# Optimization experiments

Hardware: AMD Instinct MI355X
Metric: run time of the kernel (lower is better)

Reference implementation:

```python
import jax, jax.numpy as jnp
import numpy as np
from jax import lax

B_, L_, D_ = 4, 2048, 256
DI, NS, DC, DTR = 512, 16, 4, 16  # d_inner=2*D, d_state, d_conv, dt_rank=ceil(D/16)
DFF = 4 * D_


def setup_inputs():
    key = jax.random.key(0)
    ks = jax.random.split(key, 20)
    rn = lambda k, s, sc=0.02: jax.random.normal(k, s, jnp.float32) * sc
    return {
        "x": jax.random.normal(ks[0], (B_, L_, D_), jnp.float32),
        "in_proj_w": rn(ks[1], (2 * DI, D_)), "in_proj_b": jnp.zeros((2 * DI,), jnp.float32),
        "conv_w": rn(ks[2], (DI, DC), 0.1), "conv_b": jnp.zeros((DI,), jnp.float32),
        "x_proj_w": rn(ks[3], (DTR + 2 * NS, DI)),
        "dt_proj_w": rn(ks[4], (DI, DTR), 0.1), "dt_proj_b": rn(ks[5], (DI,), 0.5),
        "A_log": jnp.log(jnp.tile(jnp.arange(1, NS + 1, dtype=jnp.float32), (DI, 1))),
        "D_ssm": jnp.ones((DI,), jnp.float32),
        "out_proj_w": rn(ks[6], (D_, DI)), "out_proj_b": jnp.zeros((D_,), jnp.float32),
        "ln1_g": jnp.ones((D_,), jnp.float32), "ln1_b": jnp.zeros((D_,), jnp.float32),
        "fc1_w": rn(ks[7], (DFF, D_)), "fc1_b": jnp.zeros((DFF,), jnp.float32),
        "fc2_w": rn(ks[8], (D_, DFF)), "fc2_b": jnp.zeros((D_,), jnp.float32),
        "ln2_g": jnp.ones((D_,), jnp.float32), "ln2_b": jnp.zeros((D_,), jnp.float32),
    }


def _layer_norm(x, g, b, eps=1e-5):
    m = jnp.mean(x, -1, keepdims=True)
    v = jnp.mean((x - m) ** 2, -1, keepdims=True)
    return (x - m) / jnp.sqrt(v + eps) * g + b


def _mamba(x, in_proj_w, in_proj_b, conv_w, conv_b, x_proj_w, dt_proj_w, dt_proj_b, A_log, D_ssm, out_proj_w, out_proj_b):
    B, L, D = x.shape
    xz = x @ in_proj_w.T + in_proj_b                       # [B,L,2*DI]
    xi, z = jnp.split(xz, 2, axis=-1)
    # causal depthwise conv over time
    xc = jnp.transpose(xi, (0, 2, 1))                       # [B,DI,L]
    xc = lax.conv_general_dilated(xc, conv_w[:, None, :], (1,), [(DC - 1, 0)],
                                  dimension_numbers=("NCH", "OIH", "NCH"),
                                  feature_group_count=DI)
    xi = jax.nn.silu(jnp.transpose(xc + conv_b[None, :, None], (0, 2, 1)))  # [B,L,DI]
    x_dbl = xi @ x_proj_w.T                                 # [B,L,DTR+2*NS]
    dt, Bs, Cs = jnp.split(x_dbl, [DTR, DTR + NS], axis=-1)
    dt = jax.nn.softplus(dt @ dt_proj_w.T + dt_proj_b)      # [B,L,DI]
    A = -jnp.exp(A_log)                                     # [DI,NS]
    dA = jnp.exp(dt[..., None] * A)                         # [B,L,DI,NS]
    dBu = dt[..., None] * Bs[:, :, None, :] * xi[..., None]  # [B,L,DI,NS]
    dA_t = jnp.moveaxis(dA, 1, 0)
    dBu_t = jnp.moveaxis(dBu, 1, 0)
    C_t = jnp.moveaxis(Cs, 1, 0)                            # [L,B,NS]

    def step(h, inp):
        a, bu, c = inp
        h = a * h + bu                                      # [B,DI,NS]
        y = jnp.einsum("bdn,bn->bd", h, c)
        return h, y

    h0 = jnp.zeros((B, DI, NS), x.dtype)
    _, ys = lax.scan(step, h0, (dA_t, dBu_t, C_t))
    y = jnp.moveaxis(ys, 0, 1) + xi * D_ssm                 # [B,L,DI]
    y = y * jax.nn.silu(z)
    return y @ out_proj_w.T + out_proj_b


def reference(x, in_proj_w, in_proj_b, conv_w, conv_b, x_proj_w, dt_proj_w, dt_proj_b,
              A_log, D_ssm, out_proj_w, out_proj_b, ln1_g, ln1_b, fc1_w, fc1_b,
              fc2_w, fc2_b, ln2_g, ln2_b):
    gelu = lambda t: jax.nn.gelu(t, approximate=False)
    ssm = _mamba(x, in_proj_w, in_proj_b, conv_w, conv_b, x_proj_w, dt_proj_w,
                 dt_proj_b, A_log, D_ssm, out_proj_w, out_proj_b)
    y = _layer_norm(x + ssm, ln1_g, ln1_b)                  # dropout = identity (eval)
    ffn = gelu(gelu(y @ fc1_w.T + fc1_b) @ fc2_w.T + fc2_b)
    return _layer_norm(y + ffn, ln2_g, ln2_b)
```

## Files before the change

kernel.cpp:

```cpp
#include <hip/hip_runtime.h>

typedef __bf16 bf16x8 __attribute__((ext_vector_type(8)));
typedef float  f32x4  __attribute__((ext_vector_type(4)));

#define AS1 __attribute__((address_space(1)))
#define AS3 __attribute__((address_space(3)))

__device__ __forceinline__ float bf2f(ushort u) {
    union { unsigned int i; float f; } v; v.i = ((unsigned int)u) << 16; return v.f;
}
__device__ __forceinline__ ushort f2bf(float f) {
    union { float f; unsigned int i; } v; v.f = f;
    unsigned int i = v.i;
    unsigned int r = i + 0x7FFFu + ((i >> 16) & 1u);
    return (ushort)(r >> 16);
}
__device__ __forceinline__ float bflo(unsigned int u) { return bf2f((ushort)(u & 0xFFFFu)); }
__device__ __forceinline__ float bfhi(unsigned int u) { return bf2f((ushort)(u >> 16)); }

__global__ void sniff_k(const ushort* __restrict__ x, int* __restrict__ flag)
{
    const int lane = threadIdx.x;
    int cnt = 0;
    #pragma unroll
    for (int r = 0; r < 4; r++) {
        const ushort u = x[lane + r * 64];
        const int e = (u >> 7) & 0xFF;
        if ((u & 0x7FFF) == 0 || (e >= 112 && e <= 141)) cnt++;
    }
    #pragma unroll
    for (int o = 32; o > 0; o >>= 1) cnt += __shfl_down(cnt, o);
    if (lane == 0) flag[0] = (cnt >= 224) ? 1 : 0;
}

struct CanonArgs {
    const void* src[20];
    int off[20];
    int total;
};

__launch_bounds__(256)
__global__ void canon_k(CanonArgs a, ushort* __restrict__ dst, const int* __restrict__ flag)
{
    const int i = blockIdx.x * 256 + threadIdx.x;
    if (i >= a.total) return;
    const int fl = flag[0];
    int s = 0;
    #pragma unroll
    for (int t = 1; t < 20; t++) if (i >= a.off[t]) s = t;
    const int li = i - a.off[s];
    ushort v;
    if (fl) v = ((const ushort*)a.src[s])[li];
    else    v = f2bf(((const float*)a.src[s])[li]);
    dst[i] = v;
}

__launch_bounds__(256)
__global__ void prep_k(const ushort* __restrict__ dtw, const ushort* __restrict__ xpw,
                       ushort* __restrict__ dtw_pad, ushort* __restrict__ xpw_pad)
{
    const int i = blockIdx.x * 256 + threadIdx.x;
    if (i < 16384) {
        const int dd = i >> 5, r = i & 31;
        dtw_pad[i] = (r < 16) ? dtw[dd * 16 + r] : (ushort)0;
    } else {
        const int j = i - 16384;
        const int r = j >> 9;
        xpw_pad[j] = (r < 48) ? xpw[j] : (ushort)0;
    }
}

template<int BM, int BN, int ACT, bool HASB, bool WF32, bool WBF16>
__launch_bounds__(256, 2)
__global__ void gemm_bt(const ushort* __restrict__ A, const ushort* __restrict__ W,
                        const ushort* __restrict__ bias,
                        float* __restrict__ Cf, ushort* __restrict__ Cb,
                        int M, int N, int K, int lda)
{
    constexpr int WMT = BM / 32;
    constexpr int WNT = BN / 32;
    __shared__ __align__(16) ushort As[BM * 32];
    __shared__ __align__(16) ushort Bs[BN * 32];
    const int tid  = threadIdx.x;
    const int wave = tid >> 6;
    const int lane = tid & 63;
    const int m0 = blockIdx.x * BM;
    const int n0 = blockIdx.y * BN;
    const int wm = (wave >> 1) * (BM / 2);
    const int wn = (wave & 1) * (BN / 2);
    const int lrow = lane & 15;
    const int quad = lane >> 4;

    f32x4 acc[WMT][WNT];
    #pragma unroll
    for (int i = 0; i < WMT; i++)
        #pragma unroll
        for (int j = 0; j < WNT; j++)
            #pragma unroll
            for (int r = 0; r < 4; r++) acc[i][j][r] = 0.f;

    for (int k0 = 0; k0 < K; k0 += 32) {
        #pragma unroll
        for (int t = 0; t < BM / 64; t++) {
            const int inst = t * 4 + wave;
            const int row  = inst * 16 + (lane >> 2);
            const int sub  = lane & 3;
            const ushort* gp = A + (size_t)(m0 + row) * lda + (k0 + sub * 8);
            __builtin_amdgcn_global_load_lds((AS1 void*)(void*)gp,
                                             (AS3 void*)(As + inst * 512), 16, 0, 0);
        }
        #pragma unroll
        for (int t = 0; t < BN / 64; t++) {
            const int inst = t * 4 + wave;
            const int row  = inst * 16 + (lane >> 2);
            const int sub  = lane & 3;
            const ushort* gp = W + (size_t)(n0 + row) * K + (k0 + sub * 8);
            __builtin_amdgcn_global_load_lds((AS1 void*)(void*)gp,
                                             (AS3 void*)(Bs + inst * 512), 16, 0, 0);
        }
        __syncthreads();

        bf16x8 afr[WMT], bfr[WNT];
        #pragma unroll
        for (int i = 0; i < WMT; i++)
            afr[i] = *(const bf16x8*)&As[(wm + i * 16 + lrow) * 32 + quad * 8];
        #pragma unroll
        for (int j = 0; j < WNT; j++)
            bfr[j] = *(const bf16x8*)&Bs[(wn + j * 16 + lrow) * 32 + quad * 8];
        #pragma unroll
        for (int i = 0; i < WMT; i++)
            #pragma unroll
            for (int j = 0; j < WNT; j++)
                acc[i][j] = __builtin_amdgcn_mfma_f32_16x16x32_bf16(afr[i], bfr[j], acc[i][j], 0, 0, 0);
        __syncthreads();
    }

    #pragma unroll
    for (int i = 0; i < WMT; i++) {
        const int gm = m0 + wm + i * 16 + quad * 4;
        #pragma unroll
        for (int j = 0; j < WNT; j++) {
            const int gn = n0 + wn + j * 16 + lrow;
            const float bv = HASB ? bf2f(bias[gn]) : 0.f;
            #pragma unroll
            for (int r = 0; r < 4; r++) {
                float v = acc[i][j][r] + bv;
                if (ACT == 1) v = 0.5f * v * (1.f + erff(v * 0.70710678118654752f));
                if (ACT == 2) v = (v > 15.f) ? v : __logf(1.f + __expf(v));
                const size_t off = (size_t)(gm + r) * N + gn;
                if (WF32)  Cf[off] = v;
                if (WBF16) Cb[off] = f2bf(v);
            }
        }
    }
}

__launch_bounds__(256)
__global__ void conv_silu_k(const ushort* __restrict__ xz, const ushort* __restrict__ cw,
                            const ushort* __restrict__ cb, ushort* __restrict__ xc)
{
    const int idx = blockIdx.x * 256 + threadIdx.x;
    const int t  = idx >> 6;
    const int d8 = (idx & 63) * 8;
    const int l  = t & 2047;

    ushort wl[32];
    *(uint4*)&wl[0]  = *(const uint4*)&cw[d8 * 4];
    *(uint4*)&wl[8]  = *(const uint4*)&cw[d8 * 4 + 8];
    *(uint4*)&wl[16] = *(const uint4*)&cw[d8 * 4 + 16];
    *(uint4*)&wl[24] = *(const uint4*)&cw[d8 * 4 + 24];

    ushort bl[8];
    *(uint4*)&bl[0] = *(const uint4*)&cb[d8];

    float acc[8];
    #pragma unroll
    for (int j = 0; j < 8; j++) acc[j] = bf2f(bl[j]);

    #pragma unroll
    for (int k = 0; k < 4; k++) {
        const int ls = l - 3 + k;
        if (ls >= 0) {
            ushort xl[8];
            *(uint4*)&xl[0] = *(const uint4*)&xz[(size_t)(t - 3 + k) * 1024 + d8];
            #pragma unroll
            for (int j = 0; j < 8; j++) acc[j] += bf2f(xl[j]) * bf2f(wl[j * 4 + k]);
        }
    }
    ushort ol[8];
    #pragma unroll
    for (int j = 0; j < 8; j++) {
        const float s = acc[j] / (1.f + __expf(-acc[j]));
        ol[j] = f2bf(s);
    }
    *(uint4*)&xc[(size_t)idx * 8] = *(uint4*)&ol[0];
}

__launch_bounds__(256)
__global__ void scan1_k(const float* __restrict__ dt, const ushort* __restrict__ xc,
                        const float* __restrict__ xdbl, const ushort* __restrict__ Alog,
                        float* __restrict__ summ)
{
    __shared__ float Bsh[32 * 16];
    const int tid = threadIdx.x;
    const int c = blockIdx.y, b = blockIdx.z;
    const int t0 = b * 2048 + c * 32;
    for (int e = tid; e < 512; e += 256)
        Bsh[e] = xdbl[(size_t)(t0 + (e >> 4)) * 64 + 16 + (e & 15)];
    __syncthreads();
    const int d = blockIdx.x * 256 + tid;
    float A[16], h[16];
    #pragma unroll
    for (int n = 0; n < 16; n++) {
        A[n] = -__expf(bf2f(Alog[d * 16 + n]));
        h[n] = 0.f;
    }
    float sdt = 0.f;
    for (int i = 0; i < 32; i++) {
        const int t = t0 + i;
        const float dtv = dt[(size_t)t * 512 + d];
        const float xiv = bf2f(xc[(size_t)t * 512 + d]);
        const float dx = dtv * xiv;
        sdt += dtv;
        const float* Br = &Bsh[i * 16];
        #pragma unroll
        for (int n = 0; n < 16; n++) {
            const float da = __expf(dtv * A[n]);
            h[n] = da * h[n] + dx * Br[n];
        }
    }
    const size_t base = ((size_t)(b * 64 + c) * 32) * 512 + d;
    #pragma unroll
    for (int n = 0; n < 16; n++) summ[base + (size_t)n * 512] = __expf(A[n] * sdt);
    #pragma unroll
    for (int n = 0; n < 16; n++) summ[base + (size_t)(16 + n) * 512] = h[n];
}

__launch_bounds__(512)
__global__ void combine_k(float* __restrict__ summ)
{
    const int b = blockIdx.x >> 4, n = blockIdx.x & 15;
    const int d = threadIdx.x;
    float h = 0.f;
    for (int c = 0; c < 64; c++) {
        const size_t sb = ((size_t)((b * 64 + c) * 32 + n)) * 512 + d;
        const float p  = summ[sb];
        const float hl = summ[sb + 8192];
        summ[sb] = h;
        h = p * h + hl;
    }
}

__launch_bounds__(256)
__global__ void scan2_k(const float* __restrict__ dt, ushort* xc,
                        const float* __restrict__ xdbl, const ushort* __restrict__ Alog,
                        const float* __restrict__ summ, const ushort* __restrict__ xz,
                        const ushort* __restrict__ Dssm)
{
    __shared__ float Bsh[32 * 16];
    __shared__ float Csh[32 * 16];
    const int tid = threadIdx.x;
    const int c = blockIdx.y, b = blockIdx.z;
    const int t0 = b * 2048 + c * 32;
    for (int e = tid; e < 512; e += 256) {
        const size_t rb = (size_t)(t0 + (e >> 4)) * 64 + (e & 15);
        Bsh[e] = xdbl[rb + 16];
        Csh[e] = xdbl[rb + 32];
    }
    __syncthreads();
    const int d = blockIdx.x * 256 + tid;
    float A[16], h[16];
    #pragma unroll
    for (int n = 0; n < 16; n++) A[n] = -__expf(bf2f(Alog[d * 16 + n]));
    const size_t base = ((size_t)(b * 64 + c) * 32) * 512 + d;
    #pragma unroll
    for (int n = 0; n < 16; n++) h[n] = summ[base + (size_t)n * 512];
    const float Dv = bf2f(Dssm[d]);
    for (int i = 0; i < 32; i++) {
        const int t = t0 + i;
        const float dtv = dt[(size_t)t * 512 + d];
        const float xiv = bf2f(xc[(size_t)t * 512 + d]);
        const float dx = dtv * xiv;
        const float* Br = &Bsh[i * 16];
        const float* Cr = &Csh[i * 16];
        float yv = 0.f;
        #pragma unroll
        for (int n = 0; n < 16; n++) {
            const float da = __expf(dtv * A[n]);
            h[n] = da * h[n] + dx * Br[n];
            yv += h[n] * Cr[n];
        }
        yv += xiv * Dv;
        const float zv = bf2f(xz[(size_t)t * 1024 + 512 + d]);
        yv *= zv / (1.f + __expf(-zv));
        xc[(size_t)t * 512 + d] = f2bf(yv);
    }
}

__launch_bounds__(256)
__global__ void ln1_k(const void* __restrict__ xin, const float* __restrict__ sout,
                      const ushort* __restrict__ g, const ushort* __restrict__ bb,
                      float* __restrict__ y1f, ushort* __restrict__ y1b,
                      const int* __restrict__ flag)
{
    const int w = threadIdx.x >> 6, l = threadIdx.x & 63;
    const int t = blockIdx.x * 4 + w;
    const size_t base = (size_t)t * 256 + l * 4;
    const int fl = flag[0];
    float v[4];
    if (fl) {
        const uint2 xr = *(const uint2*)((const ushort*)xin + base);
        v[0] = bflo(xr.x); v[1] = bfhi(xr.x); v[2] = bflo(xr.y); v[3] = bfhi(xr.y);
    } else {
        const float4 xr = *(const float4*)((const float*)xin + base);
        v[0] = xr.x; v[1] = xr.y; v[2] = xr.z; v[3] = xr.w;
    }
    const float4 sv = *(const float4*)&sout[base];
    v[0] += sv.x; v[1] += sv.y; v[2] += sv.z; v[3] += sv.w;
    float s = v[0] + v[1] + v[2] + v[3];
    #pragma unroll
    for (int o = 32; o > 0; o >>= 1) s += __shfl_xor(s, o);
    const float mean = s * (1.f / 256.f);
    float q = 0.f;
    #pragma unroll
    for (int j = 0; j < 4; j++) { const float dv = v[j] - mean; q += dv * dv; }
    #pragma unroll
    for (int o = 32; o > 0; o >>= 1) q += __shfl_xor(q, o);
    const float r = rsqrtf(q * (1.f / 256.f) + 1e-5f);
    const uint2 gv = *(const uint2*)&g[l * 4];
    const uint2 bv = *(const uint2*)&bb[l * 4];
    const float gf[4] = { bflo(gv.x), bfhi(gv.x), bflo(gv.y), bfhi(gv.y) };
    const float bf[4] = { bflo(bv.x), bfhi(bv.x), bflo(bv.y), bfhi(bv.y) };
    float4 of;
    float* op = (float*)&of;
    ushort ob[4];
    #pragma unroll
    for (int j = 0; j < 4; j++) {
        const float o2 = (v[j] - mean) * r * gf[j] + bf[j];
        op[j] = o2; ob[j] = f2bf(o2);
    }
    *(float4*)&y1f[base] = of;
    *(uint2*)&y1b[base] = *(uint2*)&ob[0];
}

__launch_bounds__(256)
__global__ void ln2_k(const float* __restrict__ y1f, const float* __restrict__ ffn,
                      const ushort* __restrict__ g, const ushort* __restrict__ bb,
                      void* __restrict__ out, const int* __restrict__ flag)
{
    const int w = threadIdx.x >> 6, l = threadIdx.x & 63;
    const int t = blockIdx.x * 4 + w;
    const size_t base = (size_t)t * 256 + l * 4;
    const int fl = flag[0];
    const float4 av = *(const float4*)&y1f[base];
    const float4 fv = *(const float4*)&ffn[base];
    float v[4] = { av.x + fv.x, av.y + fv.y, av.z + fv.z, av.w + fv.w };
    float s = v[0] + v[1] + v[2] + v[3];
    #pragma unroll
    for (int o = 32; o > 0; o >>= 1) s += __shfl_xor(s, o);
    const float mean = s * (1.f / 256.f);
    float q = 0.f;
    #pragma unroll
    for (int j = 0; j < 4; j++) { const float dv = v[j] - mean; q += dv * dv; }
    #pragma unroll
    for (int o = 32; o > 0; o >>= 1) q += __shfl_xor(q, o);
    const float r = rsqrtf(q * (1.f / 256.f) + 1e-5f);
    const uint2 gv = *(const uint2*)&g[l * 4];
    const uint2 bv = *(const uint2*)&bb[l * 4];
    const float gf[4] = { bflo(gv.x), bfhi(gv.x), bflo(gv.y), bfhi(gv.y) };
    const float bf[4] = { bflo(bv.x), bfhi(bv.x), bflo(bv.y), bfhi(bv.y) };
    if (fl) {
        ushort ob[4];
        #pragma unroll
        for (int j = 0; j < 4; j++) ob[j] = f2bf((v[j] - mean) * r * gf[j] + bf[j]);
        *(uint2*)((ushort*)out + base) = *(uint2*)&ob[0];
    } else {
        float4 of;
        float* op = (float*)&of;
        #pragma unroll
        for (int j = 0; j < 4; j++) op[j] = (v[j] - mean) * r * gf[j] + bf[j];
        *(float4*)((float*)out + base) = of;
    }
}

extern "C" void kernel_launch(void* const* d_in, const int* in_sizes, int n_in,
                              void* d_out, int out_size, void* d_ws, size_t ws_size,
                              hipStream_t stream)
{
    char* ws = (char*)d_ws;
    int*    flag  = (int*)(ws + 0);
    ushort* canon = (ushort*)(ws + 256);

    static const int coff[20] = {
        0,        2097152,  2359296,  2360320,  2362368,
        2362880,  2387456,  2395648,  2396160,  2404352,
        2404864,  2535936,  2536192,  2536448,  2536704,
        2798848,  2799872,  3062016,  3062272,  3062528 };
    static const int ctot = 3062784;

    CanonArgs ca;
    for (int i = 0; i < 20; i++) { ca.src[i] = d_in[i]; ca.off[i] = coff[i]; }
    ca.total = ctot;

    const ushort* cx   = canon + coff[0];
    const ushort* cipw = canon + coff[1];
    const ushort* cipb = canon + coff[2];
    const ushort* ccw  = canon + coff[3];
    const ushort* ccb  = canon + coff[4];
    const ushort* cxpw = canon + coff[5];
    const ushort* cdtw = canon + coff[6];
    const ushort* cdtb = canon + coff[7];
    const ushort* calog= canon + coff[8];
    const ushort* cdssm= canon + coff[9];
    const ushort* copw = canon + coff[10];
    const ushort* copb = canon + coff[11];
    const ushort* cln1g= canon + coff[12];
    const ushort* cln1b= canon + coff[13];
    const ushort* cf1w = canon + coff[14];
    const ushort* cf1b = canon + coff[15];
    const ushort* cf2w = canon + coff[16];
    const ushort* cf2b = canon + coff[17];
    const ushort* cln2g= canon + coff[18];
    const ushort* cln2b= canon + coff[19];

    ushort* xpw_pad = (ushort*)(ws + 6291456);
    ushort* dtw_pad = (ushort*)(ws + 6356992);
    ushort* xz      = (ushort*)(ws + 8388608);
    ushort* xc      = (ushort*)(ws + 25165824);
    float*  xdbl_f  = (float*)(ws + 33554432);
    ushort* xdbl_b  = (ushort*)(ws + 35651584);
    float*  dt      = (float*)(ws + 36700160);
    float*  summ    = (float*)(ws + 53477376);
    float*  sout = (float*)(ws + 8388608);
    float*  y1f  = (float*)(ws + 16777216);
    ushort* y1b  = (ushort*)(ws + 33554432);
    ushort* f1   = (ushort*)(ws + 37748736);
    float*  ffn  = (float*)(ws + 54525952);
    ushort* yb   = xc;

    sniff_k<<<1, 64, 0, stream>>>((const ushort*)d_in[0], flag);
    canon_k<<<(ctot + 255) / 256, 256, 0, stream>>>(ca, canon, flag);
    prep_k<<<192, 256, 0, stream>>>(cdtw, cxpw, dtw_pad, xpw_pad);

    gemm_bt<128, 128, 0, true, false, true><<<dim3(64, 8), 256, 0, stream>>>(
        cx, cipw, cipb, nullptr, xz, 8192, 1024, 256, 256);
    conv_silu_k<<<2048, 256, 0, stream>>>(xz, ccw, ccb, xc);
    gemm_bt<64, 64, 0, false, true, true><<<dim3(128, 1), 256, 0, stream>>>(
        xc, xpw_pad, nullptr, xdbl_f, xdbl_b, 8192, 64, 512, 512);
    gemm_bt<128, 64, 2, true, true, false><<<dim3(64, 8), 256, 0, stream>>>(
        xdbl_b, dtw_pad, cdtb, dt, nullptr, 8192, 512, 32, 64);
    scan1_k<<<dim3(2, 64, 4), 256, 0, stream>>>(dt, xc, xdbl_f, calog, summ);
    combine_k<<<64, 512, 0, stream>>>(summ);
    scan2_k<<<dim3(2, 64, 4), 256, 0, stream>>>(dt, xc, xdbl_f, calog, summ, xz, cdssm);
    gemm_bt<128, 64, 0, true, true, false><<<dim3(64, 4), 256, 0, stream>>>(
        yb, copw, copb, sout, nullptr, 8192, 256, 512, 512);
    ln1_k<<<2048, 256, 0, stream>>>(d_in[0], sout, cln1g, cln1b, y1f, y1b, flag);
    gemm_bt<128, 128, 1, true, false, true><<<dim3(64, 8), 256, 0, stream>>>(
        y1b, cf1w, cf1b, nullptr, f1, 8192, 1024, 256, 256);
    gemm_bt<128, 64, 1, true, true, false><<<dim3(64, 4), 256, 0, stream>>>(
        f1, cf2w, cf2b, ffn, nullptr, 8192, 256, 1024, 1024);
    ln2_k<<<2048, 256, 0, stream>>>(y1f, ffn, cln2g, cln2b, d_out, flag);
}
```

Measured before the change: 268.3 us.

## Fuse dt projection into scans, LayerNorms into GEMMs, and drop prep kernels

The dt projection and softplus are now computed inside both scan kernels from the x_dbl rows staged in shared memory, which removes the dt GEMM and its large fp32 dt buffer round-trip. The out_proj and fc2 GEMMs get a new full-row (BN=256) variant that adds the residual and applies LayerNorm in the epilogue, replacing the separate ln1/ln2 kernels and the sout/ffn buffers. The sniff and prep kernels are folded into canon_k, which now computes the dtype check per thread and writes the padded x_proj weights directly. In exchange, the dt projection is computed twice (once per scan pass), the LayerNorm GEMMs run on only 128 blocks, and variance now uses the single-pass E[x²]-mean² formula.

```diff
diff --git a/kernel.cpp b/kernel.cpp
--- a/kernel.cpp
+++ b/kernel.cpp
@@ -18,9 +18,8 @@
 __device__ __forceinline__ float bflo(unsigned int u) { return bf2f((ushort)(u & 0xFFFFu)); }
 __device__ __forceinline__ float bfhi(unsigned int u) { return bf2f((ushort)(u >> 16)); }
 
-__global__ void sniff_k(const ushort* __restrict__ x, int* __restrict__ flag)
-{
-    const int lane = threadIdx.x;
+__device__ __forceinline__ bool sniff_inline(const ushort* __restrict__ x) {
+    const int lane = threadIdx.x & 63;
     int cnt = 0;
     #pragma unroll
     for (int r = 0; r < 4; r++) {
@@ -29,8 +28,8 @@
         if ((u & 0x7FFF) == 0 || (e >= 112 && e <= 141)) cnt++;
     }
     #pragma unroll
-    for (int o = 32; o > 0; o >>= 1) cnt += __shfl_down(cnt, o);
-    if (lane == 0) flag[0] = (cnt >= 224) ? 1 : 0;
+    for (int o = 32; o > 0; o >>= 1) cnt += __shfl_xor(cnt, o);
+    return cnt >= 224;
 }
 
 struct CanonArgs {
@@ -40,11 +39,16 @@
 };
 
 __launch_bounds__(256)
-__global__ void canon_k(CanonArgs a, ushort* __restrict__ dst, const int* __restrict__ flag)
+__global__ void canon_k(CanonArgs a, ushort* __restrict__ dst, ushort* __restrict__ xpw_pad,
+                        const ushort* __restrict__ sniffx)
 {
     const int i = blockIdx.x * 256 + threadIdx.x;
-    if (i >= a.total) return;
-    const int fl = flag[0];
+    if (i >= a.total) {
+        const int j = i - a.total;
+        if (j < 8192) xpw_pad[24576 + j] = 0;
+        return;
+    }
+    const bool fl = sniff_inline(sniffx);
     int s = 0;
     #pragma unroll
     for (int t = 1; t < 20; t++) if (i >= a.off[t]) s = t;
@@ -53,21 +57,7 @@
     if (fl) v = ((const ushort*)a.src[s])[li];
     else    v = f2bf(((const float*)a.src[s])[li]);
     dst[i] = v;
-}
-
-__launch_bounds__(256)
-__global__ void prep_k(const ushort* __restrict__ dtw, const ushort* __restrict__ xpw,
-                       ushort* __restrict__ dtw_pad, ushort* __restrict__ xpw_pad)
-{
-    const int i = blockIdx.x * 256 + threadIdx.x;
-    if (i < 16384) {
-        const int dd = i >> 5, r = i & 31;
-        dtw_pad[i] = (r < 16) ? dtw[dd * 16 + r] : (ushort)0;
-    } else {
-        const int j = i - 16384;
-        const int r = j >> 9;
-        xpw_pad[j] = (r < 48) ? xpw[j] : (ushort)0;
-    }
+    if (s == 5) xpw_pad[li] = v;
 }
 
 template<int BM, int BN, int ACT, bool HASB, bool WF32, bool WBF16>
@@ -146,10 +136,155 @@
             for (int r = 0; r < 4; r++) {
                 float v = acc[i][j][r] + bv;
                 if (ACT == 1) v = 0.5f * v * (1.f + erff(v * 0.70710678118654752f));
-                if (ACT == 2) v = (v > 15.f) ? v : __logf(1.f + __expf(v));
                 const size_t off = (size_t)(gm + r) * N + gn;
                 if (WF32)  Cf[off] = v;
                 if (WBF16) Cb[off] = f2bf(v);
+            }
+        }
+    }
+}
+
+template<int ACT, int MODE>
+__launch_bounds__(256, 2)
+__global__ void gemm_ln(const ushort* __restrict__ A, const ushort* __restrict__ W,
+                        const ushort* __restrict__ bias,
+                        const void* __restrict__ resid, const ushort* __restrict__ sniffx,
+                        const ushort* __restrict__ g, const ushort* __restrict__ bvec,
+                        float* __restrict__ y1f_out, ushort* __restrict__ y1b_out,
+                        void* __restrict__ dout, int K)
+{
+    __shared__ __align__(16) ushort As[64 * 32];
+    __shared__ __align__(16) ushort Bs[256 * 32];
+    __shared__ float redS[128], redQ[128];
+    const int tid  = threadIdx.x;
+    const int wave = tid >> 6;
+    const int lane = tid & 63;
+    const int m0 = blockIdx.x * 64;
+    const int wm = (wave >> 1) * 32;
+    const int wn = (wave & 1) * 128;
+    const int lrow = lane & 15;
+    const int quad = lane >> 4;
+
+    f32x4 acc[2][8];
+    #pragma unroll
+    for (int i = 0; i < 2; i++)
+        #pragma unroll
+        for (int j = 0; j < 8; j++)
+            #pragma unroll
+            for (int r = 0; r < 4; r++) acc[i][j][r] = 0.f;
+
+    for (int k0 = 0; k0 < K; k0 += 32) {
+        {
+            const int row = wave * 16 + (lane >> 2);
+            const int sub = lane & 3;
+            const ushort* gp = A + (size_t)(m0 + row) * K + (k0 + sub * 8);
+            __builtin_amdgcn_global_load_lds((AS1 void*)(void*)gp,
+                                             (AS3 void*)(As + wave * 512), 16, 0, 0);
+        }
+        #pragma unroll
+        for (int t = 0; t < 4; t++) {
+            const int inst = t * 4 + wave;
+            const int row  = inst * 16 + (lane >> 2);
+            const int sub  = lane & 3;
+            const ushort* gp = W + (size_t)row * K + (k0 + sub * 8);
+            __builtin_amdgcn_global_load_lds((AS1 void*)(void*)gp,
+                                             (AS3 void*)(Bs + inst * 512), 16, 0, 0);
+        }
+        __syncthreads();
+
+        bf16x8 afr[2], bfr[8];
+        #pragma unroll
+        for (int i = 0; i < 2; i++)
+            afr[i] = *(const bf16x8*)&As[(wm + i * 16 + lrow) * 32 + quad * 8];
+        #pragma unroll
+        for (int j = 0; j < 8; j++)
+            bfr[j] = *(const bf16x8*)&Bs[(wn + j * 16 + lrow) * 32 + quad * 8];
+        #pragma unroll
+        for (int i = 0; i < 2; i++)
+            #pragma unroll
+            for (int j = 0; j < 8; j++)
+                acc[i][j] = __builtin_amdgcn_mfma_f32_16x16x32_bf16(afr[i], bfr[j], acc[i][j], 0, 0, 0);
+        __syncthreads();
+    }
+
+    const bool fl = sniff_inline(sniffx);
+    float bv[8];
+    #pragma unroll
+    for (int j = 0; j < 8; j++) bv[j] = bf2f(bias[wn + j * 16 + lrow]);
+
+    float ps[2][4], pq[2][4];
+    #pragma unroll
+    for (int i = 0; i < 2; i++)
+        #pragma unroll
+        for (int r = 0; r < 4; r++) { ps[i][r] = 0.f; pq[i][r] = 0.f; }
+
+    #pragma unroll
+    for (int i = 0; i < 2; i++) {
+        const int gm = m0 + wm + i * 16 + quad * 4;
+        #pragma unroll
+        for (int j = 0; j < 8; j++) {
+            const int col = wn + j * 16 + lrow;
+            #pragma unroll
+            for (int r = 0; r < 4; r++) {
+                const size_t off = (size_t)(gm + r) * 256 + col;
+                float v = acc[i][j][r] + bv[j];
+                if (ACT == 1) v = 0.5f * v * (1.f + erff(v * 0.70710678118654752f));
+                float rv;
+                if (MODE == 0) rv = fl ? bf2f(((const ushort*)resid)[off])
+                                       : ((const float*)resid)[off];
+                else           rv = ((const float*)resid)[off];
+                v += rv;
+                acc[i][j][r] = v;
+                ps[i][r] += v;
+                pq[i][r] += v * v;
+            }
+        }
+    }
+    #pragma unroll
+    for (int i = 0; i < 2; i++)
+        #pragma unroll
+        for (int r = 0; r < 4; r++) {
+            float s = ps[i][r], q = pq[i][r];
+            #pragma unroll
+            for (int o = 8; o > 0; o >>= 1) { s += __shfl_xor(s, o); q += __shfl_xor(q, o); }
+            if (lrow == 0) {
+                const int lr = wm + i * 16 + quad * 4 + r;
+                redS[(wave & 1) * 64 + lr] = s;
+                redQ[(wave & 1) * 64 + lr] = q;
+            }
+        }
+    __syncthreads();
+
+    float gf[8], bf2v[8];
+    #pragma unroll
+    for (int j = 0; j < 8; j++) {
+        const int col = wn + j * 16 + lrow;
+        gf[j]   = bf2f(g[col]);
+        bf2v[j] = bf2f(bvec[col]);
+    }
+    #pragma unroll
+    for (int i = 0; i < 2; i++) {
+        const int gm = m0 + wm + i * 16 + quad * 4;
+        #pragma unroll
+        for (int r = 0; r < 4; r++) {
+            const int lr = wm + i * 16 + quad * 4 + r;
+            const float S = redS[lr] + redS[64 + lr];
+            const float Q = redQ[lr] + redQ[64 + lr];
+            const float mean = S * (1.f / 256.f);
+            const float var  = Q * (1.f / 256.f) - mean * mean;
+            const float rs   = rsqrtf(var + 1e-5f);
+            #pragma unroll
+            for (int j = 0; j < 8; j++) {
+                const int col = wn + j * 16 + lrow;
+                const size_t off = (size_t)(gm + r) * 256 + col;
+                const float out = (acc[i][j][r] - mean) * rs * gf[j] + bf2v[j];
+                if (MODE == 0) {
+                    y1f_out[off] = out;
+                    y1b_out[off] = f2bf(out);
+                } else {
+                    if (fl) ((ushort*)dout)[off] = f2bf(out);
+                    else    ((float*)dout)[off]  = out;
+                }
             }
         }
     }
@@ -197,18 +332,27 @@
 }
 
 __launch_bounds__(256)
-__global__ void scan1_k(const float* __restrict__ dt, const ushort* __restrict__ xc,
-                        const float* __restrict__ xdbl, const ushort* __restrict__ Alog,
-                        float* __restrict__ summ)
-{
-    __shared__ float Bsh[32 * 16];
+__global__ void scan1_k(const float* __restrict__ xdbl, const ushort* __restrict__ xc,
+                        const ushort* __restrict__ dtw, const ushort* __restrict__ dtb,
+                        const ushort* __restrict__ Alog, float* __restrict__ summ)
+{
+    __shared__ float XD[32 * 32];
     const int tid = threadIdx.x;
     const int c = blockIdx.y, b = blockIdx.z;
     const int t0 = b * 2048 + c * 32;
-    for (int e = tid; e < 512; e += 256)
-        Bsh[e] = xdbl[(size_t)(t0 + (e >> 4)) * 64 + 16 + (e & 15)];
+    for (int e = tid; e < 1024; e += 256)
+        XD[e] = xdbl[(size_t)(t0 + (e >> 5)) * 64 + (e & 31)];
     __syncthreads();
     const int d = blockIdx.x * 256 + tid;
+
+    const uint4 w0 = *(const uint4*)&dtw[d * 16];
+    const uint4 w1 = *(const uint4*)&dtw[d * 16 + 8];
+    const float wd[16] = { bflo(w0.x), bfhi(w0.x), bflo(w0.y), bfhi(w0.y),
+                           bflo(w0.z), bfhi(w0.z), bflo(w0.w), bfhi(w0.w),
+                           bflo(w1.x), bfhi(w1.x), bflo(w1.y), bfhi(w1.y),
+                           bflo(w1.z), bfhi(w1.z), bflo(w1.w), bfhi(w1.w) };
+    const float dtbv = bf2f(dtb[d]);
+
     float A[16], h[16];
     #pragma unroll
     for (int n = 0; n < 16; n++) {
@@ -218,15 +362,18 @@
     float sdt = 0.f;
     for (int i = 0; i < 32; i++) {
         const int t = t0 + i;
-        const float dtv = dt[(size_t)t * 512 + d];
+        const float* Xr = &XD[i * 32];
+        float s = dtbv;
+        #pragma unroll
+        for (int k = 0; k < 16; k++) s += Xr[k] * wd[k];
+        const float dtv = (s > 15.f) ? s : __logf(1.f + __expf(s));
         const float xiv = bf2f(xc[(size_t)t * 512 + d]);
         const float dx = dtv * xiv;
         sdt += dtv;
-        const float* Br = &Bsh[i * 16];
         #pragma unroll
         for (int n = 0; n < 16; n++) {
             const float da = __expf(dtv * A[n]);
-            h[n] = da * h[n] + dx * Br[n];
+            h[n] = da * h[n] + dx * Xr[16 + n];
         }
     }
     const size_t base = ((size_t)(b * 64 + c) * 32) * 512 + d;
@@ -252,23 +399,28 @@
 }
 
 __launch_bounds__(256)
-__global__ void scan2_k(const float* __restrict__ dt, ushort* xc,
-                        const float* __restrict__ xdbl, const ushort* __restrict__ Alog,
-                        const float* __restrict__ summ, const ushort* __restrict__ xz,
-                        const ushort* __restrict__ Dssm)
-{
-    __shared__ float Bsh[32 * 16];
-    __shared__ float Csh[32 * 16];
+__global__ void scan2_k(const float* __restrict__ xdbl, ushort* xc,
+                        const ushort* __restrict__ dtw, const ushort* __restrict__ dtb,
+                        const ushort* __restrict__ Alog, const float* __restrict__ summ,
+                        const ushort* __restrict__ xz, const ushort* __restrict__ Dssm)
+{
+    __shared__ float XD[32 * 48];
     const int tid = threadIdx.x;
     const int c = blockIdx.y, b = blockIdx.z;
     const int t0 = b * 2048 + c * 32;
-    for (int e = tid; e < 512; e += 256) {
-        const size_t rb = (size_t)(t0 + (e >> 4)) * 64 + (e & 15);
-        Bsh[e] = xdbl[rb + 16];
-        Csh[e] = xdbl[rb + 32];
-    }
+    for (int e = tid; e < 1536; e += 256)
+        XD[e] = xdbl[(size_t)(t0 + (e / 48)) * 64 + (e % 48)];
     __syncthreads();
     const int d = blockIdx.x * 256 + tid;
+
+    const uint4 w0 = *(const uint4*)&dtw[d * 16];
+    const uint4 w1 = *(const uint4*)&dtw[d * 16 + 8];
+    const float wd[16] = { bflo(w0.x), bfhi(w0.x), bflo(w0.y), bfhi(w0.y),
+                           bflo(w0.z), bfhi(w0.z), bflo(w0.w), bfhi(w0.w),
+                           bflo(w1.x), bfhi(w1.x), bflo(w1.y), bfhi(w1.y),
+                           bflo(w1.z), bfhi(w1.z), bflo(w1.w), bfhi(w1.w) };
+    const float dtbv = bf2f(dtb[d]);
+
     float A[16], h[16];
     #pragma unroll
     for (int n = 0; n < 16; n++) A[n] = -__expf(bf2f(Alog[d * 16 + n]));
@@ -276,19 +428,22 @@
     #pragma unroll
     for (int n = 0; n < 16; n++) h[n] = summ[base + (size_t)n * 512];
     const float Dv = bf2f(Dssm[d]);
+
     for (int i = 0; i < 32; i++) {
         const int t = t0 + i;
-        const float dtv = dt[(size_t)t * 512 + d];
+        const float* Xr = &XD[i * 48];
+        float s = dtbv;
+        #pragma unroll
+        for (int k = 0; k < 16; k++) s += Xr[k] * wd[k];
+        const float dtv = (s > 15.f) ? s : __logf(1.f + __expf(s));
         const float xiv = bf2f(xc[(size_t)t * 512 + d]);
         const float dx = dtv * xiv;
-        const float* Br = &Bsh[i * 16];
-        const float* Cr = &Csh[i * 16];
         float yv = 0.f;
         #pragma unroll
         for (int n = 0; n < 16; n++) {
             const float da = __expf(dtv * A[n]);
-            h[n] = da * h[n] + dx * Br[n];
-            yv += h[n] * Cr[n];
+            h[n] = da * h[n] + dx * Xr[16 + n];
+            yv += h[n] * Xr[32 + n];
         }
         yv += xiv * Dv;
         const float zv = bf2f(xz[(size_t)t * 1024 + 512 + d]);
@@ -297,98 +452,11 @@
     }
 }
 
-__launch_bounds__(256)
-__global__ void ln1_k(const void* __restrict__ xin, const float* __restrict__ sout,
-                      const ushort* __restrict__ g, const ushort* __restrict__ bb,
-                      float* __restrict__ y1f, ushort* __restrict__ y1b,
-                      const int* __restrict__ flag)
-{
-    const int w = threadIdx.x >> 6, l = threadIdx.x & 63;
-    const int t = blockIdx.x * 4 + w;
-    const size_t base = (size_t)t * 256 + l * 4;
-    const int fl = flag[0];
-    float v[4];
-    if (fl) {
-        const uint2 xr = *(const uint2*)((const ushort*)xin + base);
-        v[0] = bflo(xr.x); v[1] = bfhi(xr.x); v[2] = bflo(xr.y); v[3] = bfhi(xr.y);
-    } else {
-        const float4 xr = *(const float4*)((const float*)xin + base);
-        v[0] = xr.x; v[1] = xr.y; v[2] = xr.z; v[3] = xr.w;
-    }
-    const float4 sv = *(const float4*)&sout[base];
-    v[0] += sv.x; v[1] += sv.y; v[2] += sv.z; v[3] += sv.w;
-    float s = v[0] + v[1] + v[2] + v[3];
-    #pragma unroll
-    for (int o = 32; o > 0; o >>= 1) s += __shfl_xor(s, o);
-    const float mean = s * (1.f / 256.f);
-    float q = 0.f;
-    #pragma unroll
-    for (int j = 0; j < 4; j++) { const float dv = v[j] - mean; q += dv * dv; }
-    #pragma unroll
-    for (int o = 32; o > 0; o >>= 1) q += __shfl_xor(q, o);
-    const float r = rsqrtf(q * (1.f / 256.f) + 1e-5f);
-    const uint2 gv = *(const uint2*)&g[l * 4];
-    const uint2 bv = *(const uint2*)&bb[l * 4];
-    const float gf[4] = { bflo(gv.x), bfhi(gv.x), bflo(gv.y), bfhi(gv.y) };
-    const float bf[4] = { bflo(bv.x), bfhi(bv.x), bflo(bv.y), bfhi(bv.y) };
-    float4 of;
-    float* op = (float*)&of;
-    ushort ob[4];
-    #pragma unroll
-    for (int j = 0; j < 4; j++) {
-        const float o2 = (v[j] - mean) * r * gf[j] + bf[j];
-        op[j] = o2; ob[j] = f2bf(o2);
-    }
-    *(float4*)&y1f[base] = of;
-    *(uint2*)&y1b[base] = *(uint2*)&ob[0];
-}
-
-__launch_bounds__(256)
-__global__ void ln2_k(const float* __restrict__ y1f, const float* __restrict__ ffn,
-                      const ushort* __restrict__ g, const ushort* __restrict__ bb,
-                      void* __restrict__ out, const int* __restrict__ flag)
-{
-    const int w = threadIdx.x >> 6, l = threadIdx.x & 63;
-    const int t = blockIdx.x * 4 + w;
-    const size_t base = (size_t)t * 256 + l * 4;
-    const int fl = flag[0];
-    const float4 av = *(const float4*)&y1f[base];
-    const float4 fv = *(const float4*)&ffn[base];
-    float v[4] = { av.x + fv.x, av.y + fv.y, av.z + fv.z, av.w + fv.w };
-    float s = v[0] + v[1] + v[2] + v[3];
-    #pragma unroll
-    for (int o = 32; o > 0; o >>= 1) s += __shfl_xor(s, o);
-    const float mean = s * (1.f / 256.f);
-    float q = 0.f;
-    #pragma unroll
-    for (int j = 0; j < 4; j++) { const float dv = v[j] - mean; q += dv * dv; }
-    #pragma unroll
-    for (int o = 32; o > 0; o >>= 1) q += __shfl_xor(q, o);
-    const float r = rsqrtf(q * (1.f / 256.f) + 1e-5f);
-    const uint2 gv = *(const uint2*)&g[l * 4];
-    const uint2 bv = *(const uint2*)&bb[l * 4];
-    const float gf[4] = { bflo(gv.x), bfhi(gv.x), bflo(gv.y), bfhi(gv.y) };
-    const float bf[4] = { bflo(bv.x), bfhi(bv.x), bflo(bv.y), bfhi(bv.y) };
-    if (fl) {
-        ushort ob[4];
-        #pragma unroll
-        for (int j = 0; j < 4; j++) ob[j] = f2bf((v[j] - mean) * r * gf[j] + bf[j]);
-        *(uint2*)((ushort*)out + base) = *(uint2*)&ob[0];
-    } else {
-        float4 of;
-        float* op = (float*)&of;
-        #pragma unroll
-        for (int j = 0; j < 4; j++) op[j] = (v[j] - mean) * r * gf[j] + bf[j];
-        *(float4*)((float*)out + base) = of;
-    }
-}
-
 extern "C" void kernel_launch(void* const* d_in, const int* in_sizes, int n_in,
                               void* d_out, int out_size, void* d_ws, size_t ws_size,
                               hipStream_t stream)
 {
     char* ws = (char*)d_ws;
-    int*    flag  = (int*)(ws + 0);
     ushort* canon = (ushort*)(ws + 256);
 
     static const int coff[20] = {
@@ -407,7 +475,6 @@
     const ushort* cipb = canon + coff[2];
     const ushort* ccw  = canon + coff[3];
     const ushort* ccb  = canon + coff[4];
-    const ushort* cxpw = canon + coff[5];
     const ushort* cdtw = canon + coff[6];
     const ushort* cdtb = canon + coff[7];
     const ushort* calog= canon + coff[8];
@@ -424,40 +491,29 @@
     const ushort* cln2b= canon + coff[19];
 
     ushort* xpw_pad = (ushort*)(ws + 6291456);
-    ushort* dtw_pad = (ushort*)(ws + 6356992);
     ushort* xz      = (ushort*)(ws + 8388608);
     ushort* xc      = (ushort*)(ws + 25165824);
     float*  xdbl_f  = (float*)(ws + 33554432);
-    ushort* xdbl_b  = (ushort*)(ws + 35651584);
-    float*  dt      = (float*)(ws + 36700160);
-    float*  summ    = (float*)(ws + 53477376);
-    float*  sout = (float*)(ws + 8388608);
-    float*  y1f  = (float*)(ws + 16777216);
-    ushort* y1b  = (ushort*)(ws + 33554432);
-    ushort* f1   = (ushort*)(ws + 37748736);
-    float*  ffn  = (float*)(ws + 54525952);
-    ushort* yb   = xc;
-
-    sniff_k<<<1, 64, 0, stream>>>((const ushort*)d_in[0], flag);
-    canon_k<<<(ctot + 255) / 256, 256, 0, stream>>>(ca, canon, flag);
-    prep_k<<<192, 256, 0, stream>>>(cdtw, cxpw, dtw_pad, xpw_pad);
-
+    float*  summ    = (float*)(ws + 35651584);
+    float*  y1f     = (float*)(ws + 52428800);
+    ushort* y1b     = (ushort*)(ws + 60817408);
+    ushort* f1      = (ushort*)(ws + 65011712);
+    ushort* yb      = xc;
+    const ushort* sx = (const ushort*)d_in[0];
+
+    canon_k<<<(ctot + 8192 + 255) / 256, 256, 0, stream>>>(ca, canon, xpw_pad, sx);
     gemm_bt<128, 128, 0, true, false, true><<<dim3(64, 8), 256, 0, stream>>>(
         cx, cipw, cipb, nullptr, xz, 8192, 1024, 256, 256);
     conv_silu_k<<<2048, 256, 0, stream>>>(xz, ccw, ccb, xc);
-    gemm_bt<64, 64, 0, false, true, true><<<dim3(128, 1), 256, 0, stream>>>(
-        xc, xpw_pad, nullptr, xdbl_f, xdbl_b, 8192, 64, 512, 512);
-    gemm_bt<128, 64, 2, true, true, false><<<dim3(64, 8), 256, 0, stream>>>(
-        xdbl_b, dtw_pad, cdtb, dt, nullptr, 8192, 512, 32, 64);
-    scan1_k<<<dim3(2, 64, 4), 256, 0, stream>>>(dt, xc, xdbl_f, calog, summ);
+    gemm_bt<64, 64, 0, false, true, false><<<dim3(128, 1), 256, 0, stream>>>(
+        xc, xpw_pad, nullptr, xdbl_f, nullptr, 8192, 64, 512, 512);
+    scan1_k<<<dim3(2, 64, 4), 256, 0, stream>>>(xdbl_f, xc, cdtw, cdtb, calog, summ);
     combine_k<<<64, 512, 0, stream>>>(summ);
-    scan2_k<<<dim3(2, 64, 4), 256, 0, stream>>>(dt, xc, xdbl_f, calog, summ, xz, cdssm);
-    gemm_bt<128, 64, 0, true, true, false><<<dim3(64, 4), 256, 0, stream>>>(
-        yb, copw, copb, sout, nullptr, 8192, 256, 512, 512);
-    ln1_k<<<2048, 256, 0, stream>>>(d_in[0], sout, cln1g, cln1b, y1f, y1b, flag);
+    scan2_k<<<dim3(2, 64, 4), 256, 0, stream>>>(xdbl_f, xc, cdtw, cdtb, calog, summ, xz, cdssm);
+    gemm_ln<0, 0><<<128, 256, 0, stream>>>(
+        yb, copw, copb, d_in[0], sx, cln1g, cln1b, y1f, y1b, nullptr, 512);
     gemm_bt<128, 128, 1, true, false, true><<<dim3(64, 8), 256, 0, stream>>>(
         y1b, cf1w, cf1b, nullptr, f1, 8192, 1024, 256, 256);
-    gemm_bt<128, 64, 1, true, true, false><<<dim3(64, 4), 256, 0, stream>>>(
-        f1, cf2w, cf2b, ffn, nullptr, 8192, 256, 1024, 1024);
-    ln2_k<<<2048, 256, 0, stream>>>(y1f, ffn, cln2g, cln2b, d_out, flag);
-}
+    gemm_ln<1, 1><<<128, 256, 0, stream>>>(
+        f1, cf2w, cf2b, y1f, sx, cln2g, cln2b, nullptr, nullptr, d_out, 1024);
+}
```

Measured after the change: 299.8 us. 1.12x slower.
